# Kernel tuning notes

Hardware: AMD Instinct MI355X
Metric: run time of the kernel (lower is better)

## Reference

```python
import jax, jax.numpy as jnp
import numpy as np
import math

B, L, D = 4, 2048, 768
N_HEADS = 12
CHUNK = 8  # query_mask=1 every CHUNK tokens -> f = B*L/CHUNK, f % B == 0
VOCAB = 50000


def setup_inputs() -> dict:
    key = jax.random.key(0)
    ks = jax.random.split(key, 8)
    scale = 1.0 / math.sqrt(D)
    x_qk = jax.random.normal(ks[0], (B, L, D), jnp.float32)
    x_v = jax.random.normal(ks[1], (B, L, D), jnp.float32)
    # deterministic query mask: feature boundary every CHUNK tokens
    pos = jnp.arange(L)
    query_mask = jnp.tile((pos % CHUNK == 0).astype(jnp.int32)[None, :], (B, 1))
    input_ids = jax.random.randint(ks[2], (B, L), 2, VOCAB).astype(jnp.int64)
    # make the last 16 tokens of each row padding to exercise the pad mask
    input_ids = input_ids.at[:, -16:].set(1)
    Wq = jax.random.normal(ks[3], (D, D), jnp.float32) * scale
    Wk = jax.random.normal(ks[4], (D, D), jnp.float32) * scale
    Wv = jax.random.normal(ks[5], (D, D), jnp.float32) * scale
    Wo = jax.random.normal(ks[6], (D, D), jnp.float32) * scale
    zb = jnp.zeros((D,), jnp.float32)
    return {"x_qk": x_qk, "x_v": x_v, "query_mask": query_mask,
            "input_ids": input_ids, "pad_token_id": 1,
            "Wq": Wq, "bq": zb, "Wk": Wk, "bk": zb,
            "Wv": Wv, "bv": zb, "Wo": Wo, "bo": zb}


def reference(x_qk, x_v, query_mask, input_ids, pad_token_id,
              Wq, bq, Wk, bk, Wv, bv, Wo, bo):
    b, l, d = x_qk.shape
    n = b * l
    qm = query_mask.reshape(-1)
    f = int(np.asarray(jnp.sum(qm)))  # static feature count (f % b == 0)
    idx = jnp.nonzero(qm == 1, size=f)[0]                     # [f] query positions
    # segment boundaries: [left_i, right_i) per feature
    left = idx
    right = jnp.concatenate([idx[1:], jnp.array([n], idx.dtype)])
    pos = jnp.arange(n)
    seg_mask = (pos[None, :] >= left[:, None]) & (pos[None, :] < right[:, None])
    seg_mask = seg_mask & (input_ids.reshape(-1) != pad_token_id)[None, :]  # [f, n]

    xq = x_qk.reshape(n, d)
    xv = x_v.reshape(n, d)
    query = xq[idx]                                           # [f, d]
    q = query @ Wq.T + bq                                     # [f, d]
    k = xq @ Wk.T + bk                                        # [n, d]
    v = xv @ Wv.T + bv                                        # [n, d]

    dh = d // N_HEADS
    qh = q.reshape(f, N_HEADS, dh).transpose(1, 0, 2)         # [h, f, dh]
    kh = k.reshape(n, N_HEADS, dh).transpose(1, 0, 2)         # [h, n, dh]
    vh = v.reshape(n, N_HEADS, dh).transpose(1, 0, 2)         # [h, n, dh]

    bias = (1.0 - seg_mask.astype(jnp.float32)) * -10000.0    # [f, n]
    scores = jnp.einsum('hfd,hnd->hfn', qh, kh) / math.sqrt(dh) + bias[None]
    attn = jax.nn.softmax(scores, axis=-1)                    # [h, f, n]
    out = jnp.einsum('hfn,hnd->hfd', attn, vh)                # [h, f, dh]
    out = out.transpose(1, 0, 2).reshape(f, d)
    out = out @ Wo.T + bo
    return out.reshape(b, f // b, d)
```

## Files before the change

### kernel.cpp

```cpp
#include <hip/hip_runtime.h>

#define DMODEL 768
#define NHEADS 12
#define MAXFULL 16
#define NSTEP 24

typedef __attribute__((ext_vector_type(8))) short short8;
typedef __attribute__((ext_vector_type(4))) float f32x4;

__device__ __forceinline__ unsigned pack2_bf16(float a, float b) {
  unsigned ua = __float_as_uint(a), ub = __float_as_uint(b);
  ua = (ua + 0x7fffu + ((ua >> 16) & 1u)) >> 16;
  ub = (ub + 0x7fffu + ((ub >> 16) & 1u)) & 0xffff0000u;
  return ua | ub;
}
__device__ __forceinline__ unsigned short bf16_1(float a) {
  unsigned ua = __float_as_uint(a);
  return (unsigned short)((ua + 0x7fffu + ((ua >> 16) & 1u)) >> 16);
}

__device__ __forceinline__ void load16_lds(const void* g, void* l) {
  __builtin_amdgcn_global_load_lds(
      (const __attribute__((address_space(1))) unsigned int*)g,
      (__attribute__((address_space(3))) unsigned int*)l, 16, 0, 0);
}

__global__ __launch_bounds__(256) void convAll(const float* __restrict__ w0,
    const float* __restrict__ w1, const float* __restrict__ w2,
    const float* __restrict__ w3, unsigned* __restrict__ o0,
    unsigned* __restrict__ o1, unsigned* __restrict__ o2,
    unsigned* __restrict__ o3, int wcount,
    const float* __restrict__ x0, const float* __restrict__ x1,
    unsigned* __restrict__ xo0, unsigned* __restrict__ xo1, int xcount) {
  const int nvw = wcount >> 2;
  const float* src[4] = {w0, w1, w2, w3};
  unsigned* dst[4] = {o0, o1, o2, o3};
  for (int idx = blockIdx.x * 256 + threadIdx.x; idx < 4 * nvw;
       idx += gridDim.x * 256) {
    int m = idx / nvw, r = idx - m * nvw;
    float4 v = ((const float4*)src[m])[r];
    dst[m][2 * r]     = pack2_bf16(v.x, v.y);
    dst[m][2 * r + 1] = pack2_bf16(v.z, v.w);
  }
  const int nvx = xcount >> 2;
  for (int idx = blockIdx.x * 256 + threadIdx.x; idx < 2 * nvx;
       idx += gridDim.x * 256) {
    int m = idx / nvx, r = idx - m * nvx;
    float4 v = m ? ((const float4*)x1)[r] : ((const float4*)x0)[r];
    unsigned* d = m ? xo1 : xo0;
    d[2 * r]     = pack2_bf16(v.x, v.y);
    d[2 * r + 1] = pack2_bf16(v.z, v.w);
  }
}

struct GSeg {
  const unsigned short* A;
  const unsigned short* W;
  const float* bias;
  const int* row_map;
  float* C;
  int base;
};

__device__ __forceinline__ void stage_step(const GSeg& d, int k0, int arow0,
    int arow1, int wrow0, int wrow1, int skc, unsigned short* AsB,
    unsigned short* BsB, int woff) {
  load16_lds(d.A + (size_t)arow0 * DMODEL + k0 + skc, AsB + woff);
  load16_lds(d.A + (size_t)arow1 * DMODEL + k0 + skc, AsB + woff + 16 * 32);
  load16_lds(d.W + (size_t)wrow0 * DMODEL + k0 + skc, BsB + woff);
  load16_lds(d.W + (size_t)wrow1 * DMODEL + k0 + skc, BsB + woff + 16 * 32);
}

__device__ __forceinline__ void compute_step(const unsigned short* AsB,
    const unsigned short* BsB, int wm, int wn, int m16, int qx,
    f32x4 acc[4][4]) {
  short8 a[4], b[4];
#pragma unroll
  for (int i = 0; i < 4; ++i)
    a[i] = *(const short8*)&AsB[(wm + i * 16 + m16) * 32 + qx * 8];
#pragma unroll
  for (int j2 = 0; j2 < 4; ++j2)
    b[j2] = *(const short8*)&BsB[(wn + j2 * 16 + m16) * 32 + qx * 8];
  __builtin_amdgcn_s_setprio(1);
#pragma unroll
  for (int i = 0; i < 4; ++i)
#pragma unroll
    for (int j2 = 0; j2 < 4; ++j2)
      acc[i][j2] = __builtin_amdgcn_mfma_f32_16x16x32_bf16(a[i], b[j2], acc[i][j2], 0, 0, 0);
  __builtin_amdgcn_s_setprio(0);
}

__global__ __launch_bounds__(256) void gemm128(GSeg g0, GSeg g1, GSeg g2) {
  __shared__ __attribute__((aligned(16))) unsigned short As[4][128 * 32];
  __shared__ __attribute__((aligned(16))) unsigned short Bs[4][128 * 32];
  const int t = threadIdx.x;
  const int id = blockIdx.x;
  const GSeg& d = (id >= g2.base) ? g2 : ((id >= g1.base) ? g1 : g0);
  const int lid = id - d.base;
  const int xcd = lid & 7, j = lid >> 3;
  const int bn = (j % 6) * 128;
  const int bm = ((j / 6) * 8 + xcd) * 128;
  const int lane = t & 63, wid = t >> 6;
  const int m16 = lane & 15, quad = lane >> 4;
  const int qx = quad ^ ((m16 >> 1) & 3);
  const int wm = (wid >> 1) * 64, wn = (wid & 1) * 64;

  f32x4 acc[4][4];
#pragma unroll
  for (int i = 0; i < 4; ++i)
#pragma unroll
    for (int j2 = 0; j2 < 4; ++j2) acc[i][j2] = (f32x4){0.f, 0.f, 0.f, 0.f};

  const int srow = wid * 32 + (lane >> 2);
  const int skc = ((lane & 3) ^ ((lane >> 3) & 3)) * 8;
  int arow0, arow1;
  if (d.row_map) {
    arow0 = d.row_map[bm + srow];
    arow1 = d.row_map[bm + srow + 16];
  } else {
    arow0 = bm + srow;
    arow1 = bm + srow + 16;
  }
  const int wrow0 = bn + srow, wrow1 = bn + srow + 16;
  const int woff = (wid * 32) * 32;

  stage_step(d, 0,  arow0, arow1, wrow0, wrow1, skc, &As[0][0], &Bs[0][0], woff);
  stage_step(d, 32, arow0, arow1, wrow0, wrow1, skc, &As[1][0], &Bs[1][0], woff);
  stage_step(d, 64, arow0, arow1, wrow0, wrow1, skc, &As[2][0], &Bs[2][0], woff);
  stage_step(d, 96, arow0, arow1, wrow0, wrow1, skc, &As[3][0], &Bs[3][0], woff);

#pragma unroll 1
  for (int g = 0; g < (NSTEP - 4) / 4; ++g) {
    const int t0 = g * 4;
#pragma unroll
    for (int u = 0; u < 4; ++u) {
      const int ts = t0 + u;
      asm volatile("s_waitcnt vmcnt(12)" ::: "memory");
      __builtin_amdgcn_s_barrier();
      __builtin_amdgcn_sched_barrier(0);
      compute_step(&As[u][0], &Bs[u][0], wm, wn, m16, qx, acc);
      __builtin_amdgcn_s_barrier();
      __builtin_amdgcn_sched_barrier(0);
      stage_step(d, (ts + 4) * 32, arow0, arow1, wrow0, wrow1, skc,
                 &As[u][0], &Bs[u][0], woff);
    }
  }
  asm volatile("s_waitcnt vmcnt(12)" ::: "memory");
  __builtin_amdgcn_s_barrier();
  __builtin_amdgcn_sched_barrier(0);
  compute_step(&As[0][0], &Bs[0][0], wm, wn, m16, qx, acc);
  asm volatile("s_waitcnt vmcnt(8)" ::: "memory");
  __builtin_amdgcn_s_barrier();
  __builtin_amdgcn_sched_barrier(0);
  compute_step(&As[1][0], &Bs[1][0], wm, wn, m16, qx, acc);
  asm volatile("s_waitcnt vmcnt(4)" ::: "memory");
  __builtin_amdgcn_s_barrier();
  __builtin_amdgcn_sched_barrier(0);
  compute_step(&As[2][0], &Bs[2][0], wm, wn, m16, qx, acc);
  asm volatile("s_waitcnt vmcnt(0)" ::: "memory");
  __builtin_amdgcn_s_barrier();
  __builtin_amdgcn_sched_barrier(0);
  compute_step(&As[3][0], &Bs[3][0], wm, wn, m16, qx, acc);

  float bv[4]; int bcol[4];
#pragma unroll
  for (int j2 = 0; j2 < 4; ++j2) {
    bcol[j2] = bn + wn + j2 * 16 + m16;
    bv[j2] = d.bias[bcol[j2]];
  }
#pragma unroll
  for (int i = 0; i < 4; ++i) {
    const int rbase = bm + wm + i * 16 + quad * 4;
#pragma unroll
    for (int r = 0; r < 4; ++r) {
      const int row = rbase + r;
#pragma unroll
      for (int j2 = 0; j2 < 4; ++j2)
        d.C[(size_t)row * DMODEL + bcol[j2]] = acc[i][j2][r] + bv[j2];
    }
  }
}

__global__ __launch_bounds__(1024) void build_segments(const int* __restrict__ qm,
    const int* __restrict__ ids, const int* __restrict__ padp,
    int n, int f, int* __restrict__ left, int* __restrict__ right,
    int* __restrict__ nvalid, int* __restrict__ fullrank,
    int* __restrict__ fullist, int* __restrict__ nfull) {
  __shared__ int cnt[1024];
  __shared__ int fullcnt;
  const int t = threadIdx.x;
  if (t == 0) fullcnt = 0;
  const int per = (n + 1023) >> 10;
  const int base = t * per;
  int c = 0;
  for (int i = 0; i < per; ++i) {
    int p = base + i;
    if (p < n && qm[p] != 0) ++c;
  }
  cnt[t] = c;
  __syncthreads();
  for (int off = 1; off < 1024; off <<= 1) {
    int v = (t >= off) ? cnt[t - off] : 0;
    __syncthreads();
    cnt[t] += v;
    __syncthreads();
  }
  int r = cnt[t] - c;
  for (int i = 0; i < per; ++i) {
    int p = base + i;
    if (p < n && qm[p] != 0) {
      if (r < f) left[r] = p;
      ++r;
    }
  }
  __syncthreads();
  const int pad = *padp;
  for (int i = t; i < f; i += 1024) {
    int L0 = left[i];
    int R0 = (i + 1 < f) ? left[i + 1] : n;
    right[i] = R0;
    int cv = 0;
    for (int p = L0; p < R0; ++p) cv += (ids[p] != pad) ? 1 : 0;
    nvalid[i] = cv;
    if (cv == 0) {
      int rk = atomicAdd(&fullcnt, 1);
      if (rk < MAXFULL) { fullist[rk] = i; fullrank[i] = rk; }
      else fullrank[i] = -1;
    } else {
      fullrank[i] = -1;
    }
  }
  __syncthreads();
  if (t == 0) *nfull = (fullcnt < MAXFULL) ? fullcnt : MAXFULL;
}

__device__ __forceinline__ float allreduce64(float x) {
#pragma unroll
  for (int m = 1; m < 64; m <<= 1) x += __shfl_xor(x, m, 64);
  return x;
}

__global__ __launch_bounds__(64) void attn_seg(const float* __restrict__ q,
    const float* __restrict__ k, const float* __restrict__ v,
    const int* __restrict__ left, const int* __restrict__ right,
    const int* __restrict__ nvalid, const int* __restrict__ ids,
    const int* __restrict__ padp, unsigned short* __restrict__ out) {
  const int feat = blockIdx.x, h = blockIdx.y, lane = threadIdx.x;
  if (nvalid[feat] == 0) return;
  const int off = h * 64 + lane;
  const int pad = *padp;
  const float qv = q[(size_t)feat * DMODEL + off];
  const int L0 = left[feat], R0 = right[feat];
  if (R0 - L0 == 8) {
    float kv[8], vv[8], s[8];
    int live[8];
#pragma unroll
    for (int p = 0; p < 8; ++p) {
      kv[p] = k[(size_t)(L0 + p) * DMODEL + off];
      vv[p] = v[(size_t)(L0 + p) * DMODEL + off];
      live[p] = (ids[L0 + p] != pad);
    }
#pragma unroll
    for (int p = 0; p < 8; ++p) s[p] = qv * kv[p];
#pragma unroll
    for (int m_ = 1; m_ < 64; m_ <<= 1)
#pragma unroll
      for (int p = 0; p < 8; ++p) s[p] += __shfl_xor(s[p], m_, 64);
    float mx = -1e30f;
#pragma unroll
    for (int p = 0; p < 8; ++p) {
      s[p] = live[p] ? s[p] * 0.125f : -1e30f;
      mx = fmaxf(mx, s[p]);
    }
    float l = 0.f, acc = 0.f;
#pragma unroll
    for (int p = 0; p < 8; ++p) {
      float w = __expf(s[p] - mx);
      l += w;
      acc += w * vv[p];
    }
    out[(size_t)feat * DMODEL + off] = bf16_1(acc / l);
    return;
  }
  float m = -1e30f, l = 0.f, acc = 0.f;
  for (int p = L0; p < R0; ++p) {
    if (ids[p] == pad) continue;
    float s = allreduce64(qv * k[(size_t)p * DMODEL + off]) * 0.125f;
    float mn = fmaxf(m, s);
    float al = __expf(m - mn);
    float w = __expf(s - mn);
    l = l * al + w;
    acc = acc * al + w * v[(size_t)p * DMODEL + off];
    m = mn;
  }
  out[(size_t)feat * DMODEL + off] = bf16_1(acc / l);
}

__global__ __launch_bounds__(256) void attn_full_part(const float* __restrict__ q,
    const float* __restrict__ k, const float* __restrict__ v,
    const int* __restrict__ fullist, const int* __restrict__ nfullp,
    int n, int P, float* __restrict__ pm, float* __restrict__ pl,
    float* __restrict__ pacc) {
  const int nfull = *nfullp;
  if (nfull == 0) return;
  const int t = threadIdx.x, lane = t & 63, wv = t >> 6;
  const int gw = blockIdx.x * 4 + wv;
  const int h = gw / P, piece = gw - h * P;
  const int pk = n / P;

  __shared__ float q_lds[8 * 64];
  __shared__ float w_lds[4][64 * 8];

  for (int idx = t; idx < 8 * 64; idx += 256) {
    int fl = idx >> 6, d = idx & 63;
    q_lds[idx] = (fl < nfull) ? q[(size_t)fullist[fl] * DMODEL + h * 64 + d] : 0.f;
  }
  __syncthreads();

  float m[8], l[8], acc[8];
#pragma unroll
  for (int f_ = 0; f_ < 8; ++f_) { m[f_] = -1e30f; l[f_] = 0.f; acc[f_] = 0.f; }

  for (int c = 0; c < pk; c += 64) {
    const int pc = piece * pk + c;
    float s[8];
#pragma unroll
    for (int f_ = 0; f_ < 8; ++f_) s[f_] = 0.f;
    const float4* kp = (const float4*)(k + (size_t)(pc + lane) * DMODEL + h * 64);
#pragma unroll 1
    for (int g = 0; g < 2; ++g) {
      float4 kv0 = kp[g * 8 + 0], kv1 = kp[g * 8 + 1], kv2 = kp[g * 8 + 2],
             kv3 = kp[g * 8 + 3], kv4 = kp[g * 8 + 4], kv5 = kp[g * 8 + 5],
             kv6 = kp[g * 8 + 6], kv7 = kp[g * 8 + 7];
      const float4* qb = (const float4*)&q_lds[g * 32];
#pragma unroll
      for (int f_ = 0; f_ < 8; ++f_) {
        float4 q0 = qb[f_ * 16 + 0], q1 = qb[f_ * 16 + 1], q2 = qb[f_ * 16 + 2],
               q3 = qb[f_ * 16 + 3], q4 = qb[f_ * 16 + 4], q5 = qb[f_ * 16 + 5],
               q6 = qb[f_ * 16 + 6], q7 = qb[f_ * 16 + 7];
        float acc0 = q0.x * kv0.x + q0.y * kv0.y + q0.z * kv0.z + q0.w * kv0.w;
        acc0 += q1.x * kv1.x + q1.y * kv1.y + q1.z * kv1.z + q1.w * kv1.w;
        acc0 += q2.x * kv2.x + q2.y * kv2.y + q2.z * kv2.z + q2.w * kv2.w;
        acc0 += q3.x * kv3.x + q3.y * kv3.y + q3.z * kv3.z + q3.w * kv3.w;
        acc0 += q4.x * kv4.x + q4.y * kv4.y + q4.z * kv4.z + q4.w * kv4.w;
        acc0 += q5.x * kv5.x + q5.y * kv5.y + q5.z * kv5.z + q5.w * kv5.w;
        acc0 += q6.x * kv6.x + q6.y * kv6.y + q6.z * kv6.z + q6.w * kv6.w;
        acc0 += q7.x * kv7.x + q7.y * kv7.y + q7.z * kv7.z + q7.w * kv7.w;
        s[f_] += acc0;
      }
    }
    float mx[8];
#pragma unroll
    for (int f_ = 0; f_ < 8; ++f_) mx[f_] = s[f_] * 0.125f;
#pragma unroll
    for (int f_ = 0; f_ < 8; ++f_) s[f_] = mx[f_];
#pragma unroll
    for (int st = 1; st < 64; st <<= 1)
#pragma unroll
      for (int f_ = 0; f_ < 8; ++f_) mx[f_] = fmaxf(mx[f_], __shfl_xor(mx[f_], st, 64));
    float alpha[8], w[8], sum[8];
#pragma unroll
    for (int f_ = 0; f_ < 8; ++f_) {
      float mn = fmaxf(m[f_], mx[f_]);
      alpha[f_] = __expf(m[f_] - mn);
      w[f_] = __expf(s[f_] - mn);
      m[f_] = mn;
      sum[f_] = w[f_];
    }
#pragma unroll
    for (int st = 1; st < 64; st <<= 1)
#pragma unroll
      for (int f_ = 0; f_ < 8; ++f_) sum[f_] += __shfl_xor(sum[f_], st, 64);
#pragma unroll
    for (int f_ = 0; f_ < 8; ++f_) l[f_] = l[f_] * alpha[f_] + sum[f_];
    *(float4*)&w_lds[wv][lane * 8]     = make_float4(w[0], w[1], w[2], w[3]);
    *(float4*)&w_lds[wv][lane * 8 + 4] = make_float4(w[4], w[5], w[6], w[7]);
#pragma unroll
    for (int f_ = 0; f_ < 8; ++f_) acc[f_] *= alpha[f_];
    const float* vb = v + (size_t)pc * DMODEL + h * 64 + lane;
#pragma unroll 4
    for (int kk = 0; kk < 64; ++kk) {
      float vd = vb[(size_t)kk * DMODEL];
      float4 wa = *(const float4*)&w_lds[wv][kk * 8];
      float4 wb = *(const float4*)&w_lds[wv][kk * 8 + 4];
      acc[0] += wa.x * vd; acc[1] += wa.y * vd; acc[2] += wa.z * vd; acc[3] += wa.w * vd;
      acc[4] += wb.x * vd; acc[5] += wb.y * vd; acc[6] += wb.z * vd; acc[7] += wb.w * vd;
    }
  }

  for (int f_ = 0; f_ < nfull; ++f_) {
    size_t idx = ((size_t)f_ * NHEADS + h) * P + piece;
    if (lane == 0) { pm[idx] = m[f_]; pl[idx] = l[f_]; }
    pacc[idx * 64 + lane] = acc[f_];
  }
}

__global__ __launch_bounds__(256) void attn_full_comb(
    const int* __restrict__ fullist, const int* __restrict__ nfullp,
    int P, const float* __restrict__ pm, const float* __restrict__ pl,
    const float* __restrict__ pacc, unsigned short* __restrict__ out) {
  const int fl = blockIdx.x, h = blockIdx.y;
  if (fl >= *nfullp) return;
  const int feat = fullist[fl];
  const int t = threadIdx.x, lane = t & 63, wv = t >> 6;
  const size_t base = ((size_t)fl * NHEADS + h) * P;

  __shared__ float s_pm[128];
  __shared__ float s_sc[128];
  __shared__ float s_red[4];
  __shared__ float s_part[4][64];

  for (int sp = t; sp < P; sp += 256) s_pm[sp] = pm[base + sp];
  __syncthreads();
  float mloc = -1e30f;
  for (int sp = t; sp < P; sp += 256) mloc = fmaxf(mloc, s_pm[sp]);
#pragma unroll
  for (int st = 1; st < 64; st <<= 1) mloc = fmaxf(mloc, __shfl_xor(mloc, st, 64));
  if (lane == 0) s_red[wv] = mloc;
  __syncthreads();
  const float M = fmaxf(fmaxf(s_red[0], s_red[1]), fmaxf(s_red[2], s_red[3]));
  __syncthreads();
  float lloc = 0.f;
  for (int sp = t; sp < P; sp += 256) {
    float sc = __expf(s_pm[sp] - M);
    s_sc[sp] = sc;
    lloc += pl[base + sp] * sc;
  }
#pragma unroll
  for (int st = 1; st < 64; st <<= 1) lloc += __shfl_xor(lloc, st, 64);
  if (lane == 0) s_red[wv] = lloc;
  __syncthreads();
  const float Lt = s_red[0] + s_red[1] + s_red[2] + s_red[3];
  float At = 0.f;
  for (int sp = wv; sp < P; sp += 4)
    At += pacc[(base + sp) * 64 + lane] * s_sc[sp];
  s_part[wv][lane] = At;
  __syncthreads();
  if (wv == 0) {
    float tot = s_part[0][lane] + s_part[1][lane] + s_part[2][lane] + s_part[3][lane];
    out[(size_t)feat * DMODEL + h * 64 + lane] = bf16_1(tot / Lt);
  }
}

extern "C" void kernel_launch(void* const* d_in, const int* in_sizes, int n_in,
                              void* d_out, int out_size, void* d_ws, size_t ws_size,
                              hipStream_t stream) {
  const float* x_qk = (const float*)d_in[0];
  const float* x_v  = (const float*)d_in[1];
  const int* qm     = (const int*)d_in[2];
  const int* ids    = (const int*)d_in[3];
  const int* padp   = (const int*)d_in[4];
  const float* Wq = (const float*)d_in[5];
  const float* bq = (const float*)d_in[6];
  const float* Wk = (const float*)d_in[7];
  const float* bk = (const float*)d_in[8];
  const float* Wv = (const float*)d_in[9];
  const float* bv = (const float*)d_in[10];
  const float* Wo = (const float*)d_in[11];
  const float* bo = (const float*)d_in[12];

  const int n = in_sizes[0] / DMODEL;
  const int f = out_size / DMODEL;

  float* kf = (float*)d_ws;
  float* vf = kf + (size_t)n * DMODEL;
  float* qf = vf + (size_t)n * DMODEL;
  unsigned short* af = (unsigned short*)(qf + (size_t)f * DMODEL);
  unsigned short* wqb = af + (size_t)f * DMODEL;
  unsigned short* wkb = wqb + DMODEL * DMODEL;
  unsigned short* wvb = wkb + DMODEL * DMODEL;
  unsigned short* wob = wvb + DMODEL * DMODEL;
  unsigned short* xqb = wob + DMODEL * DMODEL;
  unsigned short* xvb = xqb + (size_t)n * DMODEL;
  int* left     = (int*)(xvb + (size_t)n * DMODEL);
  int* right    = left + f;
  int* nvalid   = right + f;
  int* fullrank = nvalid + f;
  int* fullist  = fullrank + f;
  int* nfull    = fullist + MAXFULL;
  size_t off_bytes = ((size_t)((char*)(nfull + 1) - (char*)d_ws) + 255) & ~(size_t)255;
  int P = 128;
  while (P > 16) {
    size_t need = (size_t)MAXFULL * NHEADS * P * 66 * sizeof(float);
    if (off_bytes + need <= ws_size && (n / P) % 64 == 0 && n % P == 0) break;
    P >>= 1;
  }
  float* pm = (float*)((char*)d_ws + off_bytes);
  float* pl = pm + (size_t)MAXFULL * NHEADS * P;
  float* pacc = pl + (size_t)MAXFULL * NHEADS * P;

  build_segments<<<1, 1024, 0, stream>>>(qm, ids, padp, n, f, left, right,
                                         nvalid, fullrank, fullist, nfull);
  convAll<<<2048, 256, 0, stream>>>(Wq, Wk, Wv, Wo, (unsigned*)wqb,
                                    (unsigned*)wkb, (unsigned*)wvb,
                                    (unsigned*)wob, DMODEL * DMODEL,
                                    x_qk, x_v, (unsigned*)xqb, (unsigned*)xvb,
                                    n * DMODEL);

  const int TKV = 6 * (n / 128);
  const int TF  = 6 * (f / 128);
  GSeg g0 = { xqb, wkb, bk, nullptr, kf, 0 };
  GSeg g1 = { xvb, wvb, bv, nullptr, vf, TKV };
  GSeg g2 = { xqb, wqb, bq, left,    qf, 2 * TKV };
  gemm128<<<2 * TKV + TF, 256, 0, stream>>>(g0, g1, g2);

  attn_seg<<<dim3(f, NHEADS), 64, 0, stream>>>(qf, kf, vf, left, right, nvalid,
                                               ids, padp, af);
  attn_full_part<<<NHEADS * P / 4, 256, 0, stream>>>(qf, kf, vf, fullist, nfull,
                                                     n, P, pm, pl, pacc);
  attn_full_comb<<<dim3(MAXFULL, NHEADS), 256, 0, stream>>>(fullist, nfull, P,
                                                            pm, pl, pacc, af);

  GSeg gout = { af, wob, bo, nullptr, (float*)d_out, 0 };
  GSeg gnull = { af, wob, bo, nullptr, (float*)d_out, 1 << 30 };
  gemm128<<<TF, 256, 0, stream>>>(gout, gnull, gnull);
}
```

Baseline: 224.7 us.

## Use 256x256-tile GEMM kernel for fused QKV projections

Adds a gemm256 kernel with 512 threads and 256x256 output tiles, double-buffered over K in steps of 64, and uses it for the K, V and Q projection GEMMs instead of the 128x128 kernel. Larger tiles raise arithmetic intensity and halve redundant global loads of the A and W operands. The old 128-tile kernel, still used for the output projection, drops from a 4-stage to a 3-stage LDS pipeline. The trade-off is fewer blocks: 96 K/V tiles plus 12 Q tiles on a GPU with 256 CUs, so parallelism drops and occupancy may suffer.

```diff
diff --git a/kernel.cpp b/kernel.cpp
--- a/kernel.cpp
+++ b/kernel.cpp
@@ -62,6 +62,128 @@
   int base;
 };
 
+typedef unsigned short LdsTile[2][256][32];
+
+__global__ __launch_bounds__(512, 2) void gemm256(GSeg g0, GSeg g1, GSeg g2) {
+  __shared__ __attribute__((aligned(16))) LdsTile As[2];
+  __shared__ __attribute__((aligned(16))) LdsTile Bs[2];
+  const int t = threadIdx.x;
+  const int id = blockIdx.x;
+  const GSeg& d = (id >= g2.base) ? g2 : ((id >= g1.base) ? g1 : g0);
+  const int lid = id - d.base;
+  const int bn = (lid % 3) * 256;
+  const int bm = (lid / 3) * 256;
+  const int lane = t & 63, wid = t >> 6;
+  const int m16 = lane & 15, quad = lane >> 4;
+  const int qx = quad ^ ((m16 >> 1) & 3);
+  const int wr = wid >> 2, wc = wid & 3;
+
+  f32x4 acc[8][4];
+#pragma unroll
+  for (int i = 0; i < 8; ++i)
+#pragma unroll
+    for (int j2 = 0; j2 < 4; ++j2) acc[i][j2] = (f32x4){0.f, 0.f, 0.f, 0.f};
+
+  const int srow = wid * 16 + (lane >> 2);
+  const int skc = ((lane & 3) ^ ((lane >> 3) & 3)) * 8;
+  int arow0, arow1;
+  if (d.row_map) {
+    arow0 = d.row_map[bm + srow];
+    arow1 = d.row_map[bm + 128 + srow];
+  } else {
+    arow0 = bm + srow;
+    arow1 = bm + 128 + srow;
+  }
+  const int wrow0 = bn + srow, wrow1 = bn + 128 + srow;
+  const int woff0 = (wid * 16) * 32;
+  const int woff1 = (128 + wid * 16) * 32;
+
+#define STAGE256(t_, Ab, Bb) do {                                          \
+    const int kk_ = (t_) * 64 + skc;                                       \
+    load16_lds(d.A + (size_t)arow0 * DMODEL + kk_,      &Ab[0][0][0] + woff0); \
+    load16_lds(d.A + (size_t)arow1 * DMODEL + kk_,      &Ab[0][0][0] + woff1); \
+    load16_lds(d.A + (size_t)arow0 * DMODEL + kk_ + 32, &Ab[1][0][0] + woff0); \
+    load16_lds(d.A + (size_t)arow1 * DMODEL + kk_ + 32, &Ab[1][0][0] + woff1); \
+    load16_lds(d.W + (size_t)wrow0 * DMODEL + kk_,      &Bb[0][0][0] + woff0); \
+    load16_lds(d.W + (size_t)wrow1 * DMODEL + kk_,      &Bb[0][0][0] + woff1); \
+    load16_lds(d.W + (size_t)wrow0 * DMODEL + kk_ + 32, &Bb[1][0][0] + woff0); \
+    load16_lds(d.W + (size_t)wrow1 * DMODEL + kk_ + 32, &Bb[1][0][0] + woff1); \
+  } while (0)
+
+#define COMPUTE256(Ab, Bb) do {                                            \
+    _Pragma("unroll")                                                      \
+    for (int ks = 0; ks < 2; ++ks) {                                       \
+      const unsigned short* Ap = &Ab[ks][0][0];                            \
+      const unsigned short* Bp = &Bb[ks][0][0];                            \
+      short8 a_[8], b_[4];                                                 \
+      _Pragma("unroll")                                                    \
+      for (int mi = 0; mi < 8; ++mi)                                       \
+        a_[mi] = *(const short8*)&Ap[(wr * 128 + mi * 16 + m16) * 32 + qx * 8]; \
+      _Pragma("unroll")                                                    \
+      for (int nj = 0; nj < 4; ++nj)                                       \
+        b_[nj] = *(const short8*)&Bp[(wc * 64 + nj * 16 + m16) * 32 + qx * 8]; \
+      __builtin_amdgcn_s_setprio(1);                                       \
+      _Pragma("unroll")                                                    \
+      for (int mi = 0; mi < 8; ++mi)                                       \
+        _Pragma("unroll")                                                  \
+        for (int nj = 0; nj < 4; ++nj)                                     \
+          acc[mi][nj] = __builtin_amdgcn_mfma_f32_16x16x32_bf16(           \
+              a_[mi], b_[nj], acc[mi][nj], 0, 0, 0);                       \
+      __builtin_amdgcn_s_setprio(0);                                       \
+    }                                                                      \
+  } while (0)
+
+  STAGE256(0, As[0], Bs[0]);
+  STAGE256(1, As[1], Bs[1]);
+
+#pragma unroll 1
+  for (int g = 0; g < 5; ++g) {
+    asm volatile("s_waitcnt vmcnt(8)" ::: "memory");
+    __builtin_amdgcn_s_barrier();
+    __builtin_amdgcn_sched_barrier(0);
+    COMPUTE256(As[0], Bs[0]);
+    __builtin_amdgcn_s_barrier();
+    __builtin_amdgcn_sched_barrier(0);
+    STAGE256(2 * g + 2, As[0], Bs[0]);
+    asm volatile("s_waitcnt vmcnt(8)" ::: "memory");
+    __builtin_amdgcn_s_barrier();
+    __builtin_amdgcn_sched_barrier(0);
+    COMPUTE256(As[1], Bs[1]);
+    __builtin_amdgcn_s_barrier();
+    __builtin_amdgcn_sched_barrier(0);
+    STAGE256(2 * g + 3, As[1], Bs[1]);
+  }
+  asm volatile("s_waitcnt vmcnt(8)" ::: "memory");
+  __builtin_amdgcn_s_barrier();
+  __builtin_amdgcn_sched_barrier(0);
+  COMPUTE256(As[0], Bs[0]);
+  asm volatile("s_waitcnt vmcnt(0)" ::: "memory");
+  __builtin_amdgcn_s_barrier();
+  __builtin_amdgcn_sched_barrier(0);
+  COMPUTE256(As[1], Bs[1]);
+
+#undef STAGE256
+#undef COMPUTE256
+
+  float bv[4]; int bcol[4];
+#pragma unroll
+  for (int nj = 0; nj < 4; ++nj) {
+    bcol[nj] = bn + wc * 64 + nj * 16 + m16;
+    bv[nj] = d.bias[bcol[nj]];
+  }
+#pragma unroll
+  for (int mi = 0; mi < 8; ++mi) {
+    const int rbase = bm + wr * 128 + mi * 16 + quad * 4;
+#pragma unroll
+    for (int r = 0; r < 4; ++r) {
+      const int row = rbase + r;
+#pragma unroll
+      for (int nj = 0; nj < 4; ++nj)
+        d.C[(size_t)row * DMODEL + bcol[nj]] = acc[mi][nj][r] + bv[nj];
+    }
+  }
+}
+
 __device__ __forceinline__ void stage_step(const GSeg& d, int k0, int arow0,
     int arow1, int wrow0, int wrow1, int skc, unsigned short* AsB,
     unsigned short* BsB, int woff) {
@@ -91,8 +213,8 @@
 }
 
 __global__ __launch_bounds__(256) void gemm128(GSeg g0, GSeg g1, GSeg g2) {
-  __shared__ __attribute__((aligned(16))) unsigned short As[4][128 * 32];
-  __shared__ __attribute__((aligned(16))) unsigned short Bs[4][128 * 32];
+  __shared__ __attribute__((aligned(16))) unsigned short As[3][128 * 32];
+  __shared__ __attribute__((aligned(16))) unsigned short Bs[3][128 * 32];
   const int t = threadIdx.x;
   const int id = blockIdx.x;
   const GSeg& d = (id >= g2.base) ? g2 : ((id >= g1.base) ? g1 : g0);
@@ -127,40 +249,35 @@
   stage_step(d, 0,  arow0, arow1, wrow0, wrow1, skc, &As[0][0], &Bs[0][0], woff);
   stage_step(d, 32, arow0, arow1, wrow0, wrow1, skc, &As[1][0], &Bs[1][0], woff);
   stage_step(d, 64, arow0, arow1, wrow0, wrow1, skc, &As[2][0], &Bs[2][0], woff);
-  stage_step(d, 96, arow0, arow1, wrow0, wrow1, skc, &As[3][0], &Bs[3][0], woff);
 
 #pragma unroll 1
-  for (int g = 0; g < (NSTEP - 4) / 4; ++g) {
-    const int t0 = g * 4;
-#pragma unroll
-    for (int u = 0; u < 4; ++u) {
+  for (int g = 0; g < (NSTEP - 3) / 3; ++g) {
+    const int t0 = g * 3;
+#pragma unroll
+    for (int u = 0; u < 3; ++u) {
       const int ts = t0 + u;
-      asm volatile("s_waitcnt vmcnt(12)" ::: "memory");
+      asm volatile("s_waitcnt vmcnt(8)" ::: "memory");
       __builtin_amdgcn_s_barrier();
       __builtin_amdgcn_sched_barrier(0);
       compute_step(&As[u][0], &Bs[u][0], wm, wn, m16, qx, acc);
       __builtin_amdgcn_s_barrier();
       __builtin_amdgcn_sched_barrier(0);
-      stage_step(d, (ts + 4) * 32, arow0, arow1, wrow0, wrow1, skc,
+      stage_step(d, (ts + 3) * 32, arow0, arow1, wrow0, wrow1, skc,
                  &As[u][0], &Bs[u][0], woff);
     }
   }
-  asm volatile("s_waitcnt vmcnt(12)" ::: "memory");
+  asm volatile("s_waitcnt vmcnt(8)" ::: "memory");
   __builtin_amdgcn_s_barrier();
   __builtin_amdgcn_sched_barrier(0);
   compute_step(&As[0][0], &Bs[0][0], wm, wn, m16, qx, acc);
-  asm volatile("s_waitcnt vmcnt(8)" ::: "memory");
+  asm volatile("s_waitcnt vmcnt(4)" ::: "memory");
   __builtin_amdgcn_s_barrier();
   __builtin_amdgcn_sched_barrier(0);
   compute_step(&As[1][0], &Bs[1][0], wm, wn, m16, qx, acc);
-  asm volatile("s_waitcnt vmcnt(4)" ::: "memory");
+  asm volatile("s_waitcnt vmcnt(0)" ::: "memory");
   __builtin_amdgcn_s_barrier();
   __builtin_amdgcn_sched_barrier(0);
   compute_step(&As[2][0], &Bs[2][0], wm, wn, m16, qx, acc);
-  asm volatile("s_waitcnt vmcnt(0)" ::: "memory");
-  __builtin_amdgcn_s_barrier();
-  __builtin_amdgcn_sched_barrier(0);
-  compute_step(&As[3][0], &Bs[3][0], wm, wn, m16, qx, acc);
 
   float bv[4]; int bcol[4];
 #pragma unroll
@@ -497,12 +614,12 @@
                                     x_qk, x_v, (unsigned*)xqb, (unsigned*)xvb,
                                     n * DMODEL);
 
-  const int TKV = 6 * (n / 128);
-  const int TF  = 6 * (f / 128);
+  const int TKV256 = 3 * (n / 256);
+  const int TF256  = 3 * (f / 256);
   GSeg g0 = { xqb, wkb, bk, nullptr, kf, 0 };
-  GSeg g1 = { xvb, wvb, bv, nullptr, vf, TKV };
-  GSeg g2 = { xqb, wqb, bq, left,    qf, 2 * TKV };
-  gemm128<<<2 * TKV + TF, 256, 0, stream>>>(g0, g1, g2);
+  GSeg g1 = { xvb, wvb, bv, nullptr, vf, TKV256 };
+  GSeg g2 = { xqb, wqb, bq, left,    qf, 2 * TKV256 };
+  gemm256<<<2 * TKV256 + TF256, 512, 0, stream>>>(g0, g1, g2);
 
   attn_seg<<<dim3(f, NHEADS), 64, 0, stream>>>(qf, kf, vf, left, right, nvalid,
                                                ids, padp, af);
@@ -511,6 +628,7 @@
   attn_full_comb<<<dim3(MAXFULL, NHEADS), 256, 0, stream>>>(fullist, nfull, P,
                                                             pm, pl, pacc, af);
 
+  const int TF  = 6 * (f / 128);
   GSeg gout = { af, wob, bo, nullptr, (float*)d_out, 0 };
   GSeg gnull = { af, wob, bo, nullptr, (float*)d_out, 1 << 30 };
   gemm128<<<TF, 256, 0, stream>>>(gout, gnull, gnull);
```

Result: faster. 219.2 us (-2.5%).
